# Performance work log

Hardware: AMD Instinct MI355X
Metric: run time of the kernel (lower is better)

The kernel has to match this reference:

```python
import jax, jax.numpy as jnp
import numpy as np

N = 50000      # nodes
E = 800000     # edges (avg degree 16)
D_IN = 128
D_H = 256
NUM_LAYERS = 5


def setup_inputs() -> dict:
    key = jax.random.key(0)
    ks = jax.random.split(key, 12)
    s_in = 1.0 / np.sqrt(D_IN)
    s_h = 1.0 / np.sqrt(D_H)
    x = jax.random.normal(ks[0], (N, D_IN), jnp.float32)
    edge_index = jax.random.randint(ks[1], (2, E), 0, N, jnp.int32)
    eps_all = jnp.zeros((NUM_LAYERS,), jnp.float32)
    # torch Linear layout: weight [out, in], y = x @ W.T + b; scaled for stability
    w0_l0 = jax.random.normal(ks[2], (D_H, D_IN), jnp.float32) * s_in
    b0_l0 = jax.random.normal(ks[3], (D_H,), jnp.float32) * 0.01
    w1_l0 = jax.random.normal(ks[4], (D_H, D_H), jnp.float32) * s_h
    b1_l0 = jax.random.normal(ks[5], (D_H,), jnp.float32) * 0.01
    w0_rest = jax.random.normal(ks[6], (4, D_H, D_H), jnp.float32) * s_h
    b0_rest = jax.random.normal(ks[7], (4, D_H), jnp.float32) * 0.01
    w1_rest = jax.random.normal(ks[8], (4, D_H, D_H), jnp.float32) * s_h
    b1_rest = jax.random.normal(ks[9], (4, D_H), jnp.float32) * 0.01
    return {"x": x, "edge_index": edge_index, "eps_all": eps_all,
            "w0_l0": w0_l0, "b0_l0": b0_l0, "w1_l0": w1_l0, "b1_l0": b1_l0,
            "w0_rest": w0_rest, "b0_rest": b0_rest, "w1_rest": w1_rest, "b1_rest": b1_rest}


def _gin_layer(x, src, dst, eps, w0, b0, w1, b1):
    # gather source-node features along edges, scatter-sum into destination nodes
    aggr = jax.ops.segment_sum(x[src], dst, num_segments=N)  # [N, d]
    h = (1.0 + eps) * x + aggr
    h = jax.nn.relu(h @ w0.T + b0)   # dropout p=0.0 -> identity
    h = h @ w1.T + b1
    return jax.nn.relu(h)            # inter-layer ReLU from the trace


def reference(x, edge_index, eps_all, w0_l0, b0_l0, w1_l0, b1_l0,
              w0_rest, b0_rest, w1_rest, b1_rest):
    src = edge_index[0]  # edge_index_j (messages come from row 0)
    dst = edge_index[1]  # edge_index_i (aggregated at row 1)
    h = _gin_layer(x, src, dst, eps_all[0], w0_l0, b0_l0, w1_l0, b1_l0)
    for i in range(4):  # layers 1..4, identical shapes
        h = _gin_layer(h, src, dst, eps_all[i + 1],
                       w0_rest[i], b0_rest[i], w1_rest[i], b1_rest[i])
    return h  # [N, D_H]
```

## Files before the change

kernel.cpp:

```cpp
#include <hip/hip_runtime.h>
#include <hip/hip_bf16.h>
#include <stdint.h>

#define D_IN 128
#define D_H 256
#define NLAYERS 5

typedef __bf16 bf16x8 __attribute__((ext_vector_type(8)));
typedef float f32x4 __attribute__((ext_vector_type(4)));
typedef unsigned short u16x8 __attribute__((ext_vector_type(8)));

#define MID_STRIDE 260

__device__ inline unsigned short bfbits(float f) {
  __hip_bfloat16 h = __float2bfloat16(f);
  unsigned short s;
  __builtin_memcpy(&s, &h, 2);
  return s;
}

__device__ inline unsigned packbf(float lo, float hi) {
  return (unsigned)bfbits(lo) | ((unsigned)bfbits(hi) << 16);
}

__device__ inline void addbf2(float& a, float& b, unsigned u) {
  a += __uint_as_float(u << 16);
  b += __uint_as_float(u & 0xffff0000u);
}

__device__ inline void addbf2s(float& a, float& b, unsigned u, float s) {
  a += s * __uint_as_float(u << 16);
  b += s * __uint_as_float(u & 0xffff0000u);
}

__global__ void conv_inputs(const float* __restrict__ x, const float* __restrict__ a,
                            const float* __restrict__ b, const float* __restrict__ c,
                            const float* __restrict__ d,
                            __hip_bfloat16* __restrict__ xb,
                            __hip_bfloat16* __restrict__ wb, int nx) {
  int gid = blockIdx.x * blockDim.x + threadIdx.x;
  if (gid < nx) {
    xb[gid] = __float2bfloat16(x[gid]);
    return;
  }
  gid -= nx;
  if (gid >= 622592) return;
  float v;
  if (gid < 32768) v = a[gid];
  else if (gid < 98304) v = b[gid - 32768];
  else if (gid < 360448) v = c[gid - 98304];
  else v = d[gid - 360448];
  wb[gid] = __float2bfloat16(v);
}

#define CSR_CHUNKS 128

__global__ __launch_bounds__(256) void hist_kernel(const int* __restrict__ ei, int E,
                                                   int* __restrict__ deg, int N) {
  const int r = blockIdx.x & 7;
  const int chunk = blockIdx.x >> 3;
  const int rsize = (N + 7) >> 3;
  const int lo = r * rsize;
  const int hi = (lo + rsize < N) ? lo + rsize : N;
  const int stride = CSR_CHUNKS * 256;
  for (int e = chunk * 256 + threadIdx.x; e < E; e += stride) {
    int d = ei[E + e];
    if (d >= lo && d < hi) atomicAdd(&deg[d], 1);
  }
}

__global__ __launch_bounds__(256) void fill_kernel(const int* __restrict__ ei, int E,
                                                   const int* __restrict__ row_start,
                                                   int* __restrict__ cursor,
                                                   int* __restrict__ csr, int N) {
  const int r = blockIdx.x & 7;
  const int chunk = blockIdx.x >> 3;
  const int rsize = (N + 7) >> 3;
  const int lo = r * rsize;
  const int hi = (lo + rsize < N) ? lo + rsize : N;
  const int stride = CSR_CHUNKS * 256;
  for (int e = chunk * 256 + threadIdx.x; e < E; e += stride) {
    int d = ei[E + e];
    if (d >= lo && d < hi) {
      int p = atomicAdd(&cursor[d], 1);
      csr[row_start[d] + p] = ei[e];
    }
  }
}

__global__ __launch_bounds__(256) void block_sums(const int* __restrict__ deg,
                                                  int* __restrict__ bsum, int N) {
  int t = threadIdx.x;
  int idx = blockIdx.x * 1024 + t * 4;
  int4 v = {0, 0, 0, 0};
  if (idx + 3 < N) v = *reinterpret_cast<const int4*>(deg + idx);
  else {
    if (idx + 0 < N) v.x = deg[idx + 0];
    if (idx + 1 < N) v.y = deg[idx + 1];
    if (idx + 2 < N) v.z = deg[idx + 2];
    if (idx + 3 < N) v.w = deg[idx + 3];
  }
  int s = v.x + v.y + v.z + v.w;
#pragma unroll
  for (int off = 32; off > 0; off >>= 1) s += __shfl_down(s, off);
  __shared__ int ws[4];
  int lane = t & 63, w = t >> 6;
  if (lane == 0) ws[w] = s;
  __syncthreads();
  if (t == 0) bsum[blockIdx.x] = ws[0] + ws[1] + ws[2] + ws[3];
}

__global__ __launch_bounds__(256) void scan_apply(const int* __restrict__ deg,
                                                  const int* __restrict__ bsum,
                                                  int* __restrict__ row_start, int N) {
  __shared__ int woff[4];
  __shared__ int boff_sh;
  int t = threadIdx.x;
  if (t < 64) {
    int v = (t < blockIdx.x) ? bsum[t] : 0;
#pragma unroll
    for (int off = 32; off > 0; off >>= 1) v += __shfl_down(v, off);
    if (t == 0) boff_sh = v;
  }
  int idx = blockIdx.x * 1024 + t * 4;
  int4 v = {0, 0, 0, 0};
  if (idx + 3 < N) v = *reinterpret_cast<const int4*>(deg + idx);
  else {
    if (idx + 0 < N) v.x = deg[idx + 0];
    if (idx + 1 < N) v.y = deg[idx + 1];
    if (idx + 2 < N) v.z = deg[idx + 2];
    if (idx + 3 < N) v.w = deg[idx + 3];
  }
  int s = v.x + v.y + v.z + v.w;
  int lane = t & 63, w = t >> 6;
  int sc = s;
#pragma unroll
  for (int off = 1; off < 64; off <<= 1) {
    int u = __shfl_up(sc, off);
    if (lane >= off) sc += u;
  }
  if (lane == 63) woff[w] = sc;
  __syncthreads();
  int boff = boff_sh;
#pragma unroll
  for (int i = 0; i < 4; ++i)
    if (i < w) boff += woff[i];
  int ex = boff + sc - s;
  if (idx + 3 < N) {
    int4 o;
    o.x = ex;
    o.y = ex + v.x;
    o.z = ex + v.x + v.y;
    o.w = ex + v.x + v.y + v.z;
    *reinterpret_cast<int4*>(row_start + idx) = o;
  } else {
    if (idx + 0 < N) row_start[idx + 0] = ex;
    if (idx + 1 < N) row_start[idx + 1] = ex + v.x;
    if (idx + 2 < N) row_start[idx + 2] = ex + v.x + v.y;
    if (idx + 3 < N) row_start[idx + 3] = ex + v.x + v.y + v.z;
  }
}

template <int D>
__global__ __launch_bounds__(256) void aggregate(const unsigned short* __restrict__ hb,
                                                 const int* __restrict__ csr,
                                                 const int* __restrict__ row_start,
                                                 const int* __restrict__ deg,
                                                 const float* __restrict__ eps_all,
                                                 int layer,
                                                 unsigned short* __restrict__ pre,
                                                 int N) {
  constexpr int PL = D / 32;
  const int half = threadIdx.x >> 5;
  const int lane = threadIdx.x & 31;
  const int node = blockIdx.x * 8 + half;
  if (node >= N) return;

  const int start = row_start[node];
  const int cnt = deg[node];
  const float epsv = 1.0f + eps_all[layer];

  float acc[PL];
#pragma unroll
  for (int j = 0; j < PL; ++j) acc[j] = 0.0f;

  if (D == 256) {
    uint4 su = *reinterpret_cast<const uint4*>(hb + (size_t)node * D + lane * 8);
    for (int base = 0; base < cnt; base += 32) {
      int m = cnt - base;
      if (m > 32) m = 32;
      int idx = (lane < m) ? csr[start + base + lane] : 0;
      int i = 0;
      for (; i + 8 <= m; i += 8) {
        uint4 q[8];
#pragma unroll
        for (int r = 0; r < 8; ++r) {
          int s = __shfl(idx, i + r, 32);
          q[r] = *reinterpret_cast<const uint4*>(hb + (size_t)s * D + lane * 8);
        }
#pragma unroll
        for (int r = 0; r < 8; ++r) {
          addbf2(acc[0], acc[1], q[r].x);
          addbf2(acc[2], acc[3], q[r].y);
          addbf2(acc[4], acc[5], q[r].z);
          addbf2(acc[6], acc[7], q[r].w);
        }
      }
      for (; i + 4 <= m; i += 4) {
        uint4 q[4];
#pragma unroll
        for (int r = 0; r < 4; ++r) {
          int s = __shfl(idx, i + r, 32);
          q[r] = *reinterpret_cast<const uint4*>(hb + (size_t)s * D + lane * 8);
        }
#pragma unroll
        for (int r = 0; r < 4; ++r) {
          addbf2(acc[0], acc[1], q[r].x);
          addbf2(acc[2], acc[3], q[r].y);
          addbf2(acc[4], acc[5], q[r].z);
          addbf2(acc[6], acc[7], q[r].w);
        }
      }
      for (; i < m; ++i) {
        int s = __shfl(idx, i, 32);
        uint4 q = *reinterpret_cast<const uint4*>(hb + (size_t)s * D + lane * 8);
        addbf2(acc[0], acc[1], q.x);
        addbf2(acc[2], acc[3], q.y);
        addbf2(acc[4], acc[5], q.z);
        addbf2(acc[6], acc[7], q.w);
      }
    }
    addbf2s(acc[0], acc[1], su.x, epsv);
    addbf2s(acc[2], acc[3], su.y, epsv);
    addbf2s(acc[4], acc[5], su.z, epsv);
    addbf2s(acc[6], acc[7], su.w, epsv);
    uint4 o;
    o.x = packbf(acc[0], acc[1]);
    o.y = packbf(acc[2], acc[3]);
    o.z = packbf(acc[4], acc[5]);
    o.w = packbf(acc[6], acc[7]);
    *reinterpret_cast<uint4*>(pre + (size_t)node * D + lane * 8) = o;
  } else {
    uint2 su = *reinterpret_cast<const uint2*>(hb + (size_t)node * D + lane * 4);
    for (int base = 0; base < cnt; base += 32) {
      int m = cnt - base;
      if (m > 32) m = 32;
      int idx = (lane < m) ? csr[start + base + lane] : 0;
      int i = 0;
      for (; i + 8 <= m; i += 8) {
        uint2 q[8];
#pragma unroll
        for (int r = 0; r < 8; ++r) {
          int s = __shfl(idx, i + r, 32);
          q[r] = *reinterpret_cast<const uint2*>(hb + (size_t)s * D + lane * 4);
        }
#pragma unroll
        for (int r = 0; r < 8; ++r) {
          addbf2(acc[0], acc[1], q[r].x);
          addbf2(acc[2], acc[3], q[r].y);
        }
      }
      for (; i + 4 <= m; i += 4) {
        uint2 q[4];
#pragma unroll
        for (int r = 0; r < 4; ++r) {
          int s = __shfl(idx, i + r, 32);
          q[r] = *reinterpret_cast<const uint2*>(hb + (size_t)s * D + lane * 4);
        }
#pragma unroll
        for (int r = 0; r < 4; ++r) {
          addbf2(acc[0], acc[1], q[r].x);
          addbf2(acc[2], acc[3], q[r].y);
        }
      }
      for (; i < m; ++i) {
        int s = __shfl(idx, i, 32);
        uint2 q = *reinterpret_cast<const uint2*>(hb + (size_t)s * D + lane * 4);
        addbf2(acc[0], acc[1], q.x);
        addbf2(acc[2], acc[3], q.y);
      }
    }
    addbf2s(acc[0], acc[1], su.x, epsv);
    addbf2s(acc[2], acc[3], su.y, epsv);
    uint2 o;
    o.x = packbf(acc[0], acc[1]);
    o.y = packbf(acc[2], acc[3]);
    *reinterpret_cast<uint2*>(pre + (size_t)node * D + lane * 4) = o;
  }
}

template <int K0, bool OUT_BF16>
__global__ __launch_bounds__(512, 2) void mlp_fused(
    const unsigned short* __restrict__ Ap, const __hip_bfloat16* __restrict__ W0p,
    const float* __restrict__ b0, const __hip_bfloat16* __restrict__ W1p,
    const float* __restrict__ b1, void* __restrict__ Outp, int Nrows) {
  __shared__ unsigned short midb[2][64 * MID_STRIDE];

  constexpr int NK0 = K0 / 32;
  constexpr int NK1 = D_H / 32;
  const int tid = threadIdx.x;
  const int wid = tid >> 6;
  const bool prod = (wid < 4);
  const int cg = wid & 3;
  const int lane = tid & 63;
  const int l15 = lane & 15;
  const int kg = lane >> 4;
  const int col0 = cg * 64;
  const int nch = (Nrows + 63) >> 6;

  bf16x8 wfr[NK1][4];
  float bv[4];
  if (prod) {
    const unsigned short* Ws = (const unsigned short*)W0p;
#pragma unroll
    for (int ct = 0; ct < 4; ++ct) {
      const unsigned short* wrow = Ws + (size_t)(col0 + ct * 16 + l15) * K0 + kg * 8;
#pragma unroll
      for (int kk = 0; kk < NK0; ++kk)
        wfr[kk][ct] = *reinterpret_cast<const bf16x8*>(wrow + kk * 32);
      bv[ct] = b0[col0 + ct * 16 + l15];
    }
  } else {
    const unsigned short* Ws = (const unsigned short*)W1p;
#pragma unroll
    for (int ct = 0; ct < 4; ++ct) {
      const unsigned short* wrow = Ws + (size_t)(col0 + ct * 16 + l15) * D_H + kg * 8;
#pragma unroll
      for (int kk = 0; kk < NK1; ++kk)
        wfr[kk][ct] = *reinterpret_cast<const bf16x8*>(wrow + kk * 32);
      bv[ct] = b1[col0 + ct * 16 + l15];
    }
  }

  auto produce = [&](int c, unsigned short* buf) {
#pragma unroll
    for (int sub = 0; sub < 2; ++sub) {
      const int r0 = (c << 6) + sub * 32;
      bf16x8 afr[NK0][2];
#pragma unroll
      for (int rt = 0; rt < 2; ++rt) {
        int row = r0 + rt * 16 + l15;
        if (row > Nrows - 1) row = Nrows - 1;
        const unsigned short* ar = Ap + (size_t)row * K0 + kg * 8;
#pragma unroll
        for (int kk = 0; kk < NK0; ++kk)
          afr[kk][rt] = *reinterpret_cast<const bf16x8*>(ar + kk * 32);
      }
      f32x4 acc[2][4];
#pragma unroll
      for (int rt = 0; rt < 2; ++rt)
#pragma unroll
        for (int ct = 0; ct < 4; ++ct) acc[rt][ct] = 0.0f;
#pragma unroll
      for (int kk = 0; kk < NK0; ++kk)
#pragma unroll
        for (int rt = 0; rt < 2; ++rt)
#pragma unroll
          for (int ct = 0; ct < 4; ++ct)
            acc[rt][ct] = __builtin_amdgcn_mfma_f32_16x16x32_bf16(
                afr[kk][rt], wfr[kk][ct], acc[rt][ct], 0, 0, 0);
#pragma unroll
      for (int ct = 0; ct < 4; ++ct) {
        int col = col0 + ct * 16 + l15;
#pragma unroll
        for (int rt = 0; rt < 2; ++rt)
#pragma unroll
          for (int i = 0; i < 4; ++i) {
            int row_l = sub * 32 + rt * 16 + kg * 4 + i;
            buf[row_l * MID_STRIDE + col] =
                bfbits(fmaxf(acc[rt][ct][i] + bv[ct], 0.0f));
          }
      }
    }
  };

  auto consume = [&](int c, const unsigned short* buf) {
#pragma unroll
    for (int sub = 0; sub < 2; ++sub) {
      const int r0 = (c << 6) + sub * 32;
      f32x4 acc[2][4];
#pragma unroll
      for (int rt = 0; rt < 2; ++rt)
#pragma unroll
        for (int ct = 0; ct < 4; ++ct) acc[rt][ct] = 0.0f;
#pragma unroll
      for (int kk = 0; kk < NK1; ++kk) {
        bf16x8 mfr[2];
#pragma unroll
        for (int rt = 0; rt < 2; ++rt)
          mfr[rt] = *reinterpret_cast<const bf16x8*>(
              buf + (sub * 32 + rt * 16 + l15) * MID_STRIDE + kk * 32 + kg * 8);
#pragma unroll
        for (int rt = 0; rt < 2; ++rt)
#pragma unroll
          for (int ct = 0; ct < 4; ++ct)
            acc[rt][ct] = __builtin_amdgcn_mfma_f32_16x16x32_bf16(
                mfr[rt], wfr[kk][ct], acc[rt][ct], 0, 0, 0);
      }
#pragma unroll
      for (int ct = 0; ct < 4; ++ct) {
        int col = col0 + ct * 16 + l15;
#pragma unroll
        for (int rt = 0; rt < 2; ++rt)
#pragma unroll
          for (int i = 0; i < 4; ++i) {
            int row = r0 + rt * 16 + kg * 4 + i;
            if (row < Nrows) {
              float v = fmaxf(acc[rt][ct][i] + bv[ct], 0.0f);
              if (OUT_BF16)
                ((__hip_bfloat16*)Outp)[(size_t)row * D_H + col] = __float2bfloat16(v);
              else
                ((float*)Outp)[(size_t)row * D_H + col] = v;
            }
          }
      }
    }
  };

  int c_pr = blockIdx.x;
  int c_co = blockIdx.x;
  int pb = 0;
  if (prod && c_pr < nch) produce(c_pr, midb[0]);
  __syncthreads();
  c_pr += gridDim.x;
  while (c_co < nch) {
    if (prod) {
      if (c_pr < nch) produce(c_pr, midb[pb ^ 1]);
    } else {
      consume(c_co, midb[pb]);
    }
    __syncthreads();
    pb ^= 1;
    c_pr += gridDim.x;
    c_co += gridDim.x;
  }
}

extern "C" void kernel_launch(void* const* d_in, const int* in_sizes, int n_in,
                              void* d_out, int out_size, void* d_ws, size_t ws_size,
                              hipStream_t stream) {
  const float* x = (const float*)d_in[0];
  const int* ei = (const int*)d_in[1];
  const float* eps_all = (const float*)d_in[2];
  const float* w0_l0 = (const float*)d_in[3];
  const float* b0_l0 = (const float*)d_in[4];
  const float* w1_l0 = (const float*)d_in[5];
  const float* b1_l0 = (const float*)d_in[6];
  const float* w0_rest = (const float*)d_in[7];
  const float* b0_rest = (const float*)d_in[8];
  const float* w1_rest = (const float*)d_in[9];
  const float* b1_rest = (const float*)d_in[10];

  const int N = in_sizes[0] / D_IN;
  const int E = in_sizes[1] / 2;
  const int NX = N * D_IN;

  char* ws = (char*)d_ws;
  const size_t node_bf = (size_t)N * D_H * sizeof(unsigned short);
  unsigned short* h = (unsigned short*)ws;
  unsigned short* pre = (unsigned short*)(ws + node_bf);
  unsigned short* xb = (unsigned short*)(ws + 2 * node_bf);
  char* p = ws + 2 * node_bf + (size_t)NX * sizeof(unsigned short);
  __hip_bfloat16* wbf = (__hip_bfloat16*)p;
  p += 622592 * sizeof(__hip_bfloat16);
  int* deg = (int*)p;
  int* cursor = deg + N;
  int* row_start = cursor + N;
  int* bsum = row_start + N;
  int* csr = bsum + 64;

  __hip_bfloat16* w0_l0_bf = wbf;
  __hip_bfloat16* w1_l0_bf = wbf + 32768;
  __hip_bfloat16* w0_rest_bf = wbf + 98304;
  __hip_bfloat16* w1_rest_bf = w0_rest_bf + 262144;

  conv_inputs<<<(NX + 622592 + 255) / 256, 256, 0, stream>>>(
      x, w0_l0, w1_l0, w0_rest, w1_rest, (__hip_bfloat16*)xb, wbf, NX);

  const int nb = (N + 1023) / 1024;
  hipMemsetAsync(deg, 0, (size_t)2 * N * sizeof(int), stream);
  hist_kernel<<<8 * CSR_CHUNKS, 256, 0, stream>>>(ei, E, deg, N);
  block_sums<<<nb, 256, 0, stream>>>(deg, bsum, N);
  scan_apply<<<nb, 256, 0, stream>>>(deg, bsum, row_start, N);
  fill_kernel<<<8 * CSR_CHUNKS, 256, 0, stream>>>(ei, E, row_start, cursor, csr, N);

  const int mlpGrid = 256;
  const int aggBlocks = (N + 7) / 8;

  for (int layer = 0; layer < NLAYERS; ++layer) {
    const __hip_bfloat16* w0 =
        (layer == 0) ? w0_l0_bf : w0_rest_bf + (size_t)(layer - 1) * 65536;
    const float* b0 = (layer == 0) ? b0_l0 : b0_rest + (size_t)(layer - 1) * 256;
    const __hip_bfloat16* w1 =
        (layer == 0) ? w1_l0_bf : w1_rest_bf + (size_t)(layer - 1) * 65536;
    const float* b1 = (layer == 0) ? b1_l0 : b1_rest + (size_t)(layer - 1) * 256;

    if (layer == 0) {
      aggregate<D_IN><<<aggBlocks, 256, 0, stream>>>(xb, csr, row_start, deg,
                                                     eps_all, layer, pre, N);
      mlp_fused<D_IN, true><<<mlpGrid, 512, 0, stream>>>(pre, w0, b0, w1, b1, h, N);
    } else {
      aggregate<D_H><<<aggBlocks, 256, 0, stream>>>(h, csr, row_start, deg,
                                                    eps_all, layer, pre, N);
      if (layer == NLAYERS - 1)
        mlp_fused<D_H, false><<<mlpGrid, 512, 0, stream>>>(pre, w0, b0, w1, b1,
                                                           d_out, N);
      else
        mlp_fused<D_H, true><<<mlpGrid, 512, 0, stream>>>(pre, w0, b0, w1, b1, h, N);
    }
  }
}
```

Baseline: 546.6 us.

## Use dynamic atomic work-stealing with 32-row chunks in fused MLP kernel

Replaces the static grid-stride chunk assignment in the producer/consumer fused MLP kernel with a global atomic work counter per layer. Chunks shrink from 64 to 32 rows, halving the shared-memory double buffer. The goal is to balance load across blocks and reduce tail imbalance. In exchange, every chunk costs one global atomic and a shared broadcast, barriers become more frequent, and the per-layer counters must be reset by a small extra kernel.

```diff
diff --git a/kernel.cpp b/kernel.cpp
--- a/kernel.cpp
+++ b/kernel.cpp
@@ -293,8 +293,10 @@
 __global__ __launch_bounds__(512, 2) void mlp_fused(
     const unsigned short* __restrict__ Ap, const __hip_bfloat16* __restrict__ W0p,
     const float* __restrict__ b0, const __hip_bfloat16* __restrict__ W1p,
-    const float* __restrict__ b1, void* __restrict__ Outp, int Nrows) {
-  __shared__ unsigned short midb[2][64 * MID_STRIDE];
+    const float* __restrict__ b1, void* __restrict__ Outp, int Nrows,
+    int* __restrict__ work_ctr) {
+  __shared__ unsigned short midb[2][32 * MID_STRIDE];
+  __shared__ int next_sh;
 
   constexpr int NK0 = K0 / 32;
   constexpr int NK1 = D_H / 32;
@@ -306,7 +308,7 @@
   const int l15 = lane & 15;
   const int kg = lane >> 4;
   const int col0 = cg * 64;
-  const int nch = (Nrows + 63) >> 6;
+  const int nch = (Nrows + 31) >> 5;
 
   bf16x8 wfr[NK1][4];
   float bv[4];
@@ -333,107 +335,106 @@
   }
 
   auto produce = [&](int c, unsigned short* buf) {
-#pragma unroll
-    for (int sub = 0; sub < 2; ++sub) {
-      const int r0 = (c << 6) + sub * 32;
-      bf16x8 afr[NK0][2];
-#pragma unroll
-      for (int rt = 0; rt < 2; ++rt) {
-        int row = r0 + rt * 16 + l15;
-        if (row > Nrows - 1) row = Nrows - 1;
-        const unsigned short* ar = Ap + (size_t)row * K0 + kg * 8;
-#pragma unroll
-        for (int kk = 0; kk < NK0; ++kk)
-          afr[kk][rt] = *reinterpret_cast<const bf16x8*>(ar + kk * 32);
-      }
-      f32x4 acc[2][4];
+    const int r0 = c << 5;
+    bf16x8 afr[NK0][2];
+#pragma unroll
+    for (int rt = 0; rt < 2; ++rt) {
+      int row = r0 + rt * 16 + l15;
+      if (row > Nrows - 1) row = Nrows - 1;
+      const unsigned short* ar = Ap + (size_t)row * K0 + kg * 8;
+#pragma unroll
+      for (int kk = 0; kk < NK0; ++kk)
+        afr[kk][rt] = *reinterpret_cast<const bf16x8*>(ar + kk * 32);
+    }
+    f32x4 acc[2][4];
+#pragma unroll
+    for (int rt = 0; rt < 2; ++rt)
+#pragma unroll
+      for (int ct = 0; ct < 4; ++ct) acc[rt][ct] = 0.0f;
+#pragma unroll
+    for (int kk = 0; kk < NK0; ++kk)
 #pragma unroll
       for (int rt = 0; rt < 2; ++rt)
 #pragma unroll
-        for (int ct = 0; ct < 4; ++ct) acc[rt][ct] = 0.0f;
-#pragma unroll
-      for (int kk = 0; kk < NK0; ++kk)
-#pragma unroll
-        for (int rt = 0; rt < 2; ++rt)
-#pragma unroll
-          for (int ct = 0; ct < 4; ++ct)
-            acc[rt][ct] = __builtin_amdgcn_mfma_f32_16x16x32_bf16(
-                afr[kk][rt], wfr[kk][ct], acc[rt][ct], 0, 0, 0);
-#pragma unroll
-      for (int ct = 0; ct < 4; ++ct) {
-        int col = col0 + ct * 16 + l15;
-#pragma unroll
-        for (int rt = 0; rt < 2; ++rt)
-#pragma unroll
-          for (int i = 0; i < 4; ++i) {
-            int row_l = sub * 32 + rt * 16 + kg * 4 + i;
-            buf[row_l * MID_STRIDE + col] =
-                bfbits(fmaxf(acc[rt][ct][i] + bv[ct], 0.0f));
+        for (int ct = 0; ct < 4; ++ct)
+          acc[rt][ct] = __builtin_amdgcn_mfma_f32_16x16x32_bf16(
+              afr[kk][rt], wfr[kk][ct], acc[rt][ct], 0, 0, 0);
+#pragma unroll
+    for (int ct = 0; ct < 4; ++ct) {
+      int col = col0 + ct * 16 + l15;
+#pragma unroll
+      for (int rt = 0; rt < 2; ++rt)
+#pragma unroll
+        for (int i = 0; i < 4; ++i) {
+          int row_l = rt * 16 + kg * 4 + i;
+          buf[row_l * MID_STRIDE + col] = bfbits(fmaxf(acc[rt][ct][i] + bv[ct], 0.0f));
+        }
+    }
+  };
+
+  auto consume = [&](int c, const unsigned short* buf) {
+    const int r0 = c << 5;
+    f32x4 acc[2][4];
+#pragma unroll
+    for (int rt = 0; rt < 2; ++rt)
+#pragma unroll
+      for (int ct = 0; ct < 4; ++ct) acc[rt][ct] = 0.0f;
+#pragma unroll
+    for (int kk = 0; kk < NK1; ++kk) {
+      bf16x8 mfr[2];
+#pragma unroll
+      for (int rt = 0; rt < 2; ++rt)
+        mfr[rt] = *reinterpret_cast<const bf16x8*>(
+            buf + (rt * 16 + l15) * MID_STRIDE + kk * 32 + kg * 8);
+#pragma unroll
+      for (int rt = 0; rt < 2; ++rt)
+#pragma unroll
+        for (int ct = 0; ct < 4; ++ct)
+          acc[rt][ct] = __builtin_amdgcn_mfma_f32_16x16x32_bf16(
+              mfr[rt], wfr[kk][ct], acc[rt][ct], 0, 0, 0);
+    }
+#pragma unroll
+    for (int ct = 0; ct < 4; ++ct) {
+      int col = col0 + ct * 16 + l15;
+#pragma unroll
+      for (int rt = 0; rt < 2; ++rt)
+#pragma unroll
+        for (int i = 0; i < 4; ++i) {
+          int row = r0 + rt * 16 + kg * 4 + i;
+          if (row < Nrows) {
+            float v = fmaxf(acc[rt][ct][i] + bv[ct], 0.0f);
+            if (OUT_BF16)
+              ((__hip_bfloat16*)Outp)[(size_t)row * D_H + col] = __float2bfloat16(v);
+            else
+              ((float*)Outp)[(size_t)row * D_H + col] = v;
           }
-      }
+        }
     }
   };
 
-  auto consume = [&](int c, const unsigned short* buf) {
-#pragma unroll
-    for (int sub = 0; sub < 2; ++sub) {
-      const int r0 = (c << 6) + sub * 32;
-      f32x4 acc[2][4];
-#pragma unroll
-      for (int rt = 0; rt < 2; ++rt)
-#pragma unroll
-        for (int ct = 0; ct < 4; ++ct) acc[rt][ct] = 0.0f;
-#pragma unroll
-      for (int kk = 0; kk < NK1; ++kk) {
-        bf16x8 mfr[2];
-#pragma unroll
-        for (int rt = 0; rt < 2; ++rt)
-          mfr[rt] = *reinterpret_cast<const bf16x8*>(
-              buf + (sub * 32 + rt * 16 + l15) * MID_STRIDE + kk * 32 + kg * 8);
-#pragma unroll
-        for (int rt = 0; rt < 2; ++rt)
-#pragma unroll
-          for (int ct = 0; ct < 4; ++ct)
-            acc[rt][ct] = __builtin_amdgcn_mfma_f32_16x16x32_bf16(
-                mfr[rt], wfr[kk][ct], acc[rt][ct], 0, 0, 0);
-      }
-#pragma unroll
-      for (int ct = 0; ct < 4; ++ct) {
-        int col = col0 + ct * 16 + l15;
-#pragma unroll
-        for (int rt = 0; rt < 2; ++rt)
-#pragma unroll
-          for (int i = 0; i < 4; ++i) {
-            int row = r0 + rt * 16 + kg * 4 + i;
-            if (row < Nrows) {
-              float v = fmaxf(acc[rt][ct][i] + bv[ct], 0.0f);
-              if (OUT_BF16)
-                ((__hip_bfloat16*)Outp)[(size_t)row * D_H + col] = __float2bfloat16(v);
-              else
-                ((float*)Outp)[(size_t)row * D_H + col] = v;
-            }
-          }
-      }
-    }
-  };
-
-  int c_pr = blockIdx.x;
-  int c_co = blockIdx.x;
+  if (tid == 0) next_sh = atomicAdd(work_ctr, 1);
+  __syncthreads();
+  int c_cur = next_sh;
+  if (prod && c_cur < nch) produce(c_cur, midb[0]);
+  if (tid == 0) next_sh = atomicAdd(work_ctr, 1);
+  __syncthreads();
   int pb = 0;
-  if (prod && c_pr < nch) produce(c_pr, midb[0]);
-  __syncthreads();
-  c_pr += gridDim.x;
-  while (c_co < nch) {
+  while (c_cur < nch) {
+    int c_nxt = next_sh;
     if (prod) {
-      if (c_pr < nch) produce(c_pr, midb[pb ^ 1]);
+      if (c_nxt < nch) produce(c_nxt, midb[pb ^ 1]);
     } else {
-      consume(c_co, midb[pb]);
-    }
+      consume(c_cur, midb[pb]);
+    }
+    if (tid == 0 && c_nxt < nch) next_sh = atomicAdd(work_ctr, 1);
     __syncthreads();
     pb ^= 1;
-    c_pr += gridDim.x;
-    c_co += gridDim.x;
-  }
+    c_cur = c_nxt;
+  }
+}
+
+__global__ void reset_ctrs(int* __restrict__ p, int n) {
+  if (threadIdx.x < n) p[threadIdx.x] = 0;
 }
 
 extern "C" void kernel_launch(void* const* d_in, const int* in_sizes, int n_in,
@@ -467,7 +468,8 @@
   int* cursor = deg + N;
   int* row_start = cursor + N;
   int* bsum = row_start + N;
-  int* csr = bsum + 64;
+  int* wctr = bsum + 64;
+  int* csr = wctr + 8;
 
   __hip_bfloat16* w0_l0_bf = wbf;
   __hip_bfloat16* w1_l0_bf = wbf + 32768;
@@ -479,6 +481,7 @@
 
   const int nb = (N + 1023) / 1024;
   hipMemsetAsync(deg, 0, (size_t)2 * N * sizeof(int), stream);
+  reset_ctrs<<<1, 64, 0, stream>>>(wctr, 8);
   hist_kernel<<<8 * CSR_CHUNKS, 256, 0, stream>>>(ei, E, deg, N);
   block_sums<<<nb, 256, 0, stream>>>(deg, bsum, N);
   scan_apply<<<nb, 256, 0, stream>>>(deg, bsum, row_start, N);
@@ -498,15 +501,17 @@
     if (layer == 0) {
       aggregate<D_IN><<<aggBlocks, 256, 0, stream>>>(xb, csr, row_start, deg,
                                                      eps_all, layer, pre, N);
-      mlp_fused<D_IN, true><<<mlpGrid, 512, 0, stream>>>(pre, w0, b0, w1, b1, h, N);
+      mlp_fused<D_IN, true><<<mlpGrid, 512, 0, stream>>>(pre, w0, b0, w1, b1, h, N,
+                                                         wctr + layer);
     } else {
       aggregate<D_H><<<aggBlocks, 256, 0, stream>>>(h, csr, row_start, deg,
                                                     eps_all, layer, pre, N);
       if (layer == NLAYERS - 1)
         mlp_fused<D_H, false><<<mlpGrid, 512, 0, stream>>>(pre, w0, b0, w1, b1,
-                                                           d_out, N);
+                                                           d_out, N, wctr + layer);
       else
-        mlp_fused<D_H, true><<<mlpGrid, 512, 0, stream>>>(pre, w0, b0, w1, b1, h, N);
-    }
-  }
-}
+        mlp_fused<D_H, true><<<mlpGrid, 512, 0, stream>>>(pre, w0, b0, w1, b1, h, N,
+                                                          wctr + layer);
+    }
+  }
+}
```

Result: faster. 518.6 us (-5.1%).
